# Optimization experiments

Hardware: AMD Instinct MI355X
Metric: run time of the kernel (lower is better)

The kernel has to match this reference:

```python
import jax, jax.numpy as jnp
import numpy as np

W, H = 256, 256          # image width (x) and height (y); image indexed [x, y] like the torch code
N = 8192                 # depth-sorted visible gaussians
TILE = 16                # tile_size default
CHUNK = 128              # gaussians composited per scan step (N % CHUNK == 0)
MIN_WEIGHT = 1e-6        # early-termination threshold from render_pixel


def setup_inputs() -> dict:
    key = jax.random.key(0)
    k1, k2, k3, k4, k5 = jax.random.split(key, 5)
    # pixel-space means, uniformly over the image
    points_xy = jax.random.uniform(k1, (N, 2), dtype=jnp.float32) * jnp.array([W, H], jnp.float32)
    # SPD inverse 2D covariances: Sigma = R diag(var) R^T, inv = R diag(1/var) R^T
    theta = jax.random.uniform(k2, (N,), dtype=jnp.float32) * (2.0 * np.pi)
    sig = jax.random.uniform(k3, (N, 2), dtype=jnp.float32, minval=1.5, maxval=8.0)
    var = sig ** 2
    ct, st = jnp.cos(theta), jnp.sin(theta)
    R = jnp.stack([jnp.stack([ct, -st], -1), jnp.stack([st, ct], -1)], -2)  # [N,2,2]
    inverse_covariance = jnp.einsum('nij,nj,nkj->nik', R, 1.0 / var, R)
    # radius = ceil(2.5 * sqrt(max eigenvalue)) as in compute_radius
    radius = jnp.ceil(2.5 * jnp.sqrt(jnp.max(var, axis=1)))
    colors = jax.random.uniform(k4, (N, 3), dtype=jnp.float32)
    opacity = jax.random.normal(k5, (N,), dtype=jnp.float32)  # pre-sigmoid logits
    return dict(points_xy=points_xy, inverse_covariance=inverse_covariance,
                radius=radius, colors=colors, opacity=opacity)


def _rasterize(points_xy, inverse_covariance, radius, colors, opacity):
    px = jnp.arange(W, dtype=jnp.float32)[:, None]   # [W,1] pixel x coords
    py = jnp.arange(H, dtype=jnp.float32)[None, :]   # [1,H] pixel y coords
    # tile origin for each pixel (tile-based culling as in render_image)
    tile_x0 = ((jnp.arange(W) // TILE) * TILE).astype(jnp.float32)[:, None]  # [W,1]
    tile_y0 = ((jnp.arange(H) // TILE) * TILE).astype(jnp.float32)[None, :]  # [1,H]
    # per-gaussian bounding boxes (preprocess)
    min_x = jnp.floor(points_xy[:, 0] - radius); max_x = jnp.ceil(points_xy[:, 0] + radius)
    min_y = jnp.floor(points_xy[:, 1] - radius); max_y = jnp.ceil(points_xy[:, 1] + radius)

    n_chunks = N // CHUNK
    def chunk(a):
        return a.reshape((n_chunks, CHUNK) + a.shape[1:])
    xs = dict(mx=chunk(points_xy[:, 0]), my=chunk(points_xy[:, 1]),
              a=chunk(inverse_covariance[:, 0, 0]), b=chunk(inverse_covariance[:, 0, 1]),
              c=chunk(inverse_covariance[:, 1, 1]),
              mnx=chunk(min_x), mxx=chunk(max_x), mny=chunk(min_y), mxy=chunk(max_y),
              col=chunk(colors), op=chunk(opacity))

    @jax.checkpoint
    def body(carry, ch):
        T, color = carry  # T: [W,H] remaining transmittance; color: [W,H,3]
        dx = px[None] - ch['mx'][:, None, None]  # [C,W,1]
        dy = py[None] - ch['my'][:, None, None]  # [C,1,H]
        # mahalanobis form d^T Sigma^{-1} d with symmetric inv cov [[a,b],[b,c]]
        q = (ch['a'][:, None, None] * dx * dx
             + 2.0 * ch['b'][:, None, None] * dx * dy
             + ch['c'][:, None, None] * dy * dy)              # [C,W,H]
        alpha = jnp.exp(-0.5 * q) * jax.nn.sigmoid(ch['op'])[:, None, None]
        # gaussian participates for a pixel iff its bbox intersects that pixel's tile
        in_tile = ((ch['mnx'][:, None, None] <= tile_x0[None] + TILE)
                   & (ch['mxx'][:, None, None] >= tile_x0[None])
                   & (ch['mny'][:, None, None] <= tile_y0[None] + TILE)
                   & (ch['mxy'][:, None, None] >= tile_y0[None]))   # [C,W,H]
        alpha = jnp.where(in_tile, alpha, 0.0)
        cum = jnp.cumprod(1.0 - alpha, axis=0)                 # inclusive prefix of (1-alpha)
        T_before = T[None] * jnp.concatenate([jnp.ones_like(cum[:1]), cum[:-1]], axis=0)
        # original: test_weight = T_before*(1-alpha); terminate (skip contribution) if < min_weight
        include = (T[None] * cum) >= MIN_WEIGHT
        contrib = jnp.where(include, T_before * alpha, 0.0)   # [C,W,H]
        color = color + jnp.einsum('cwh,cd->whd', contrib, ch['col'])
        return (T * cum[-1], color), None

    init = (jnp.ones((W, H), jnp.float32), jnp.zeros((W, H, 3), jnp.float32))
    (_, color), _ = jax.lax.scan(body, init, xs)
    return color  # [W,H,3] image indexed [x,y]


def reference(points_xy, inverse_covariance, radius, colors, opacity):
    return _rasterize(points_xy, inverse_covariance, radius, colors, opacity)
```

## Files before the change

kernel.cpp:

```cpp
#include <hip/hip_runtime.h>

#define WIDTH   256
#define HEIGHT  256
#define NG      8192
#define TILE_SZ 16
#define MINW    1e-6f
#define NBATCH  32
#define CHUNK   256

__global__ __launch_bounds__(256) void raster_kernel(
    const float* __restrict__ pts,
    const float* __restrict__ icov,
    const float* __restrict__ rad,
    const float* __restrict__ cols,
    const float* __restrict__ opac,
    float* __restrict__ out)
{
    __shared__ unsigned long long s_ball[NBATCH * 4];
    __shared__ int s_pfx[2][NBATCH * 4];
    __shared__ unsigned short s_list[NG];
    __shared__ float4 s_g[CHUNK * 3];

    const int tid  = threadIdx.x;
    const int lane = tid & 63;
    const int wave = tid >> 6;
    const float tx0 = (float)(blockIdx.x * TILE_SZ);
    const float ty0 = (float)(blockIdx.y * TILE_SZ);
    const float tx1 = tx0 + (float)TILE_SZ;
    const float ty1 = ty0 + (float)TILE_SZ;

    unsigned int hitbits = 0;
    for (int b = 0; b < NBATCH; ++b) {
        const int g = b * 256 + tid;
        const float2 p = ((const float2*)pts)[g];
        const float  r = rad[g];
        bool hit = (floorf(p.x - r) <= tx1) & (ceilf(p.x + r) >= tx0)
                 & (floorf(p.y - r) <= ty1) & (ceilf(p.y + r) >= ty0);
        unsigned long long m = __ballot(hit);
        if (lane == 0) s_ball[b * 4 + wave] = m;
        if (hit) hitbits |= (1u << b);
    }
    __syncthreads();

    if (tid < 128) s_pfx[0][tid] = __popcll(s_ball[tid]);
    __syncthreads();
    int src = 0;
    for (int d = 1; d < 128; d <<= 1) {
        if (tid < 128) {
            int v = s_pfx[src][tid];
            if (tid >= d) v += s_pfx[src][tid - d];
            s_pfx[src ^ 1][tid] = v;
        }
        __syncthreads();
        src ^= 1;
    }
    const int count = s_pfx[src][127];

    {
        unsigned int hb = hitbits;
        const unsigned long long ltmask = (lane == 63) ? ~0ull >> 1 : (1ull << lane) - 1ull;
        while (hb) {
            const int b = __ffs(hb) - 1;  hb &= hb - 1;
            const int idx = b * 4 + wave;
            const unsigned long long m = s_ball[idx];
            const int base = (idx == 0) ? 0 : s_pfx[src][idx - 1];
            s_list[base + __popcll(m & ltmask)] = (unsigned short)(b * 256 + tid);
        }
    }
    __syncthreads();

    const int lx = tid >> 4, ly = tid & 15;
    const float fx = tx0 + (float)lx;
    const float fy = ty0 + (float)ly;
    float T = 1.0f, accr = 0.0f, accg = 0.0f, accb = 0.0f;
    const float kc = -0.72134752044f;

    for (int base = 0; base < count; base += CHUNK) {
        const int n = min(CHUNK, count - base);
        if (tid < n) {
            const int g = s_list[base + tid];
            const float2 p = ((const float2*)pts)[g];
            const float4 ic = ((const float4*)icov)[g];
            const float op = 1.0f / (1.0f + __expf(-opac[g]));
            s_g[tid * 3 + 0] = make_float4(p.x, p.y, kc * ic.x, 2.0f * kc * ic.y);
            s_g[tid * 3 + 1] = make_float4(kc * ic.w, op, cols[3 * g], cols[3 * g + 1]);
            s_g[tid * 3 + 2] = make_float4(cols[3 * g + 2], 0.f, 0.f, 0.f);
        }
        __syncthreads();

        for (int j0 = 0; j0 < n; j0 += 32) {
            if (__ballot(T >= MINW) == 0ull) break;
            const int jend = min(j0 + 32, n);
            #pragma unroll 8
            for (int j = j0; j < jend; ++j) {
                const float4 g0 = s_g[j * 3 + 0];
                const float4 g1 = s_g[j * 3 + 1];
                const float cbv = s_g[j * 3 + 2].x;
                const float dx = fx - g0.x;
                const float dy = fy - g0.y;
                const float q  = (g0.z * dx) * dx + (g0.w * dx) * dy + (g1.x * dy) * dy;
                const float alpha = g1.y * __builtin_amdgcn_exp2f(q);
                const float Tn = T * (1.0f - alpha);
                const float w  = (Tn >= MINW) ? T * alpha : 0.0f;
                accr = fmaf(w, g1.z, accr);
                accg = fmaf(w, g1.w, accg);
                accb = fmaf(w, cbv, accb);
                T = Tn;
            }
        }
        if (__syncthreads_count(T < MINW) == 256) break;
    }

    const int x = blockIdx.x * TILE_SZ + lx;
    const int y = blockIdx.y * TILE_SZ + ly;
    const int o = (x * HEIGHT + y) * 3;
    out[o] = accr;  out[o + 1] = accg;  out[o + 2] = accb;
}

extern "C" void kernel_launch(void* const* d_in, const int* in_sizes, int n_in,
                              void* d_out, int out_size, void* d_ws, size_t ws_size,
                              hipStream_t stream) {
    const float* pts  = (const float*)d_in[0];
    const float* icov = (const float*)d_in[1];
    const float* rad  = (const float*)d_in[2];
    const float* cols = (const float*)d_in[3];
    const float* opac = (const float*)d_in[4];
    float* out = (float*)d_out;
    dim3 grid(WIDTH / TILE_SZ, HEIGHT / TILE_SZ);
    raster_kernel<<<grid, dim3(256), 0, stream>>>(pts, icov, rad, cols, opac, out);
}
```

Baseline: 90.61 us.

## Split gaussian list into four segments per pixel with two-pass transmittance scan

Raises the block to 1024 threads so each pixel gets four threads, each handling a 64-gaussian segment of a 256-gaussian round. A first pass computes per-segment transmittance products, which are exchanged through shared memory to give each segment its starting transmittance. A second pass then composites that segment, and the partial colors are summed at the end. Red and green are packed as half2 to shrink the per-gaussian record to two float4s. This adds parallelism for the serial per-pixel loop but evaluates every exp twice, loses fine-grained early exit, and stores colors at reduced precision.

```diff
diff --git a/kernel.cpp b/kernel.cpp
--- a/kernel.cpp
+++ b/kernel.cpp
@@ -1,14 +1,19 @@
 #include <hip/hip_runtime.h>
+#include <hip/hip_fp16.h>
 
 #define WIDTH   256
 #define HEIGHT  256
 #define NG      8192
 #define TILE_SZ 16
 #define MINW    1e-6f
-#define NBATCH  32
-#define CHUNK   256
+#define BLK     1024
+#define NBATCH  (NG / BLK)
+#define NWAVE   (BLK / 64)
+#define NSEG    4
+#define SEGSZ   64
+#define ROUND   (NSEG * SEGSZ)
 
-__global__ __launch_bounds__(256) void raster_kernel(
+__global__ __launch_bounds__(BLK) void raster_kernel(
     const float* __restrict__ pts,
     const float* __restrict__ icov,
     const float* __restrict__ rad,
@@ -16,14 +21,18 @@
     const float* __restrict__ opac,
     float* __restrict__ out)
 {
-    __shared__ unsigned long long s_ball[NBATCH * 4];
-    __shared__ int s_pfx[2][NBATCH * 4];
+    __shared__ unsigned long long s_ball[NBATCH * NWAVE];
+    __shared__ int s_pfx[2][NBATCH * NWAVE];
     __shared__ unsigned short s_list[NG];
-    __shared__ float4 s_g[CHUNK * 3];
+    __shared__ float4 s_g[ROUND * 2];
+    __shared__ float s_P[NSEG][256];
+    __shared__ float s_red[NSEG][256][3];
 
     const int tid  = threadIdx.x;
     const int lane = tid & 63;
     const int wave = tid >> 6;
+    const int seg  = tid >> 8;
+    const int px   = tid & 255;
     const float tx0 = (float)(blockIdx.x * TILE_SZ);
     const float ty0 = (float)(blockIdx.y * TILE_SZ);
     const float tx1 = tx0 + (float)TILE_SZ;
@@ -31,17 +40,16 @@
 
     unsigned int hitbits = 0;
     for (int b = 0; b < NBATCH; ++b) {
-        const int g = b * 256 + tid;
+        const int g = b * BLK + tid;
         const float2 p = ((const float2*)pts)[g];
         const float  r = rad[g];
         bool hit = (floorf(p.x - r) <= tx1) & (ceilf(p.x + r) >= tx0)
                  & (floorf(p.y - r) <= ty1) & (ceilf(p.y + r) >= ty0);
         unsigned long long m = __ballot(hit);
-        if (lane == 0) s_ball[b * 4 + wave] = m;
+        if (lane == 0) s_ball[b * NWAVE + wave] = m;
         if (hit) hitbits |= (1u << b);
     }
     __syncthreads();
-
     if (tid < 128) s_pfx[0][tid] = __popcll(s_ball[tid]);
     __syncthreads();
     int src = 0;
@@ -55,66 +63,101 @@
         src ^= 1;
     }
     const int count = s_pfx[src][127];
-
     {
         unsigned int hb = hitbits;
-        const unsigned long long ltmask = (lane == 63) ? ~0ull >> 1 : (1ull << lane) - 1ull;
+        const unsigned long long ltmask = (1ull << lane) - 1ull;
         while (hb) {
             const int b = __ffs(hb) - 1;  hb &= hb - 1;
-            const int idx = b * 4 + wave;
+            const int idx = b * NWAVE + wave;
             const unsigned long long m = s_ball[idx];
-            const int base = (idx == 0) ? 0 : s_pfx[src][idx - 1];
-            s_list[base + __popcll(m & ltmask)] = (unsigned short)(b * 256 + tid);
+            const int bs = (idx == 0) ? 0 : s_pfx[src][idx - 1];
+            s_list[bs + __popcll(m & ltmask)] = (unsigned short)(b * BLK + tid);
         }
     }
     __syncthreads();
 
-    const int lx = tid >> 4, ly = tid & 15;
-    const float fx = tx0 + (float)lx;
-    const float fy = ty0 + (float)ly;
+    const float fx = tx0 + (float)(px >> 4);
+    const float fy = ty0 + (float)(px & 15);
+    const float kc = -0.72134752044f;
     float T = 1.0f, accr = 0.0f, accg = 0.0f, accb = 0.0f;
-    const float kc = -0.72134752044f;
+    const int s0 = seg * SEGSZ;
 
-    for (int base = 0; base < count; base += CHUNK) {
-        const int n = min(CHUNK, count - base);
+    for (int base = 0; base < count; base += ROUND) {
+        const int n = min(ROUND, count - base);
         if (tid < n) {
             const int g = s_list[base + tid];
             const float2 p = ((const float2*)pts)[g];
             const float4 ic = ((const float4*)icov)[g];
             const float op = 1.0f / (1.0f + __expf(-opac[g]));
-            s_g[tid * 3 + 0] = make_float4(p.x, p.y, kc * ic.x, 2.0f * kc * ic.y);
-            s_g[tid * 3 + 1] = make_float4(kc * ic.w, op, cols[3 * g], cols[3 * g + 1]);
-            s_g[tid * 3 + 2] = make_float4(cols[3 * g + 2], 0.f, 0.f, 0.f);
+            const __half2 h = __floats2half2_rn(cols[3 * g], cols[3 * g + 1]);
+            unsigned rgbits; __builtin_memcpy(&rgbits, &h, 4);
+            s_g[tid * 2 + 0] = make_float4(p.x, p.y, kc * ic.x, 2.0f * kc * ic.y);
+            s_g[tid * 2 + 1] = make_float4(kc * ic.w, op, __uint_as_float(rgbits),
+                                           cols[3 * g + 2]);
         }
         __syncthreads();
 
-        for (int j0 = 0; j0 < n; j0 += 32) {
-            if (__ballot(T >= MINW) == 0ull) break;
-            const int jend = min(j0 + 32, n);
+        float P = 1.0f;
+        if (__ballot(T >= MINW) != 0ull) {
             #pragma unroll 8
-            for (int j = j0; j < jend; ++j) {
-                const float4 g0 = s_g[j * 3 + 0];
-                const float4 g1 = s_g[j * 3 + 1];
-                const float cbv = s_g[j * 3 + 2].x;
-                const float dx = fx - g0.x;
-                const float dy = fy - g0.y;
-                const float q  = (g0.z * dx) * dx + (g0.w * dx) * dy + (g1.x * dy) * dy;
-                const float alpha = g1.y * __builtin_amdgcn_exp2f(q);
-                const float Tn = T * (1.0f - alpha);
-                const float w  = (Tn >= MINW) ? T * alpha : 0.0f;
-                accr = fmaf(w, g1.z, accr);
-                accg = fmaf(w, g1.w, accg);
-                accb = fmaf(w, cbv, accb);
-                T = Tn;
+            for (int i = 0; i < SEGSZ; ++i) {
+                const int idx = s0 + i;
+                const float4 g0 = s_g[idx * 2 + 0];
+                const float4 g1 = s_g[idx * 2 + 1];
+                const float dx = fx - g0.x, dy = fy - g0.y;
+                const float q = (g0.z * dx) * dx + (g0.w * dx) * dy + (g1.x * dy) * dy;
+                const float a = (idx < n) ? g1.y * __builtin_amdgcn_exp2f(q) : 0.0f;
+                P *= (1.0f - a);
             }
         }
-        if (__syncthreads_count(T < MINW) == 256) break;
+        s_P[seg][px] = P;
+        __syncthreads();
+
+        const float p0 = s_P[0][px], p1 = s_P[1][px], p2 = s_P[2][px], p3 = s_P[3][px];
+        float Tin = T;
+        if (seg > 0) Tin *= p0;
+        if (seg > 1) Tin *= p1;
+        if (seg > 2) Tin *= p2;
+        const float Tnext = (((T * p0) * p1) * p2) * p3;
+
+        if (__ballot(Tin >= MINW) != 0ull) {
+            float Tl = Tin;
+            #pragma unroll 8
+            for (int i = 0; i < SEGSZ; ++i) {
+                const int idx = s0 + i;
+                const float4 g0 = s_g[idx * 2 + 0];
+                const float4 g1 = s_g[idx * 2 + 1];
+                const float dx = fx - g0.x, dy = fy - g0.y;
+                const float q = (g0.z * dx) * dx + (g0.w * dx) * dy + (g1.x * dy) * dy;
+                const float a = (idx < n) ? g1.y * __builtin_amdgcn_exp2f(q) : 0.0f;
+                const float Tn = Tl * (1.0f - a);
+                const float w  = (Tn >= MINW) ? Tl * a : 0.0f;
+                const unsigned rgbits = __float_as_uint(g1.z);
+                __half2 h; __builtin_memcpy(&h, &rgbits, 4);
+                const float2 rg = __half22float2(h);
+                accr = fmaf(w, rg.x, accr);
+                accg = fmaf(w, rg.y, accg);
+                accb = fmaf(w, g1.w, accb);
+                Tl = Tn;
+            }
+        }
+        T = Tnext;
+        if (__syncthreads_count(T < MINW) == BLK) break;
     }
 
-    const int x = blockIdx.x * TILE_SZ + lx;
-    const int y = blockIdx.y * TILE_SZ + ly;
-    const int o = (x * HEIGHT + y) * 3;
-    out[o] = accr;  out[o + 1] = accg;  out[o + 2] = accb;
+    s_red[seg][px][0] = accr;
+    s_red[seg][px][1] = accg;
+    s_red[seg][px][2] = accb;
+    __syncthreads();
+    if (tid < 256) {
+        const float r = s_red[0][tid][0] + s_red[1][tid][0] + s_red[2][tid][0] + s_red[3][tid][0];
+        const float g = s_red[0][tid][1] + s_red[1][tid][1] + s_red[2][tid][1] + s_red[3][tid][1];
+        const float b = s_red[0][tid][2] + s_red[1][tid][2] + s_red[2][tid][2] + s_red[3][tid][2];
+        const int x = blockIdx.x * TILE_SZ + (tid >> 4);
+        const int y = blockIdx.y * TILE_SZ + (tid & 15);
+        const int o = (x * HEIGHT + y) * 3;
+        out[o] = r;  out[o + 1] = g;  out[o + 2] = b;
+    }
 }
 
 extern "C" void kernel_launch(void* const* d_in, const int* in_sizes, int n_in,
@@ -127,5 +170,5 @@
     const float* opac = (const float*)d_in[4];
     float* out = (float*)d_out;
     dim3 grid(WIDTH / TILE_SZ, HEIGHT / TILE_SZ);
-    raster_kernel<<<grid, dim3(256), 0, stream>>>(pts, icov, rad, cols, opac, out);
+    raster_kernel<<<grid, dim3(BLK), 0, stream>>>(pts, icov, rad, cols, opac, out);
 }
```

Measured after the change: 100.6 us. 11.0% more time.
